# Optimization experiments

Measured on AMD Instinct MI355X. Metric: run time of the kernel, lower is better.

The kernel has to match this reference:

```python
import jax, jax.numpy as jnp
import numpy as np

EMBED_DIM = 1024
NUM_HEADS = 16
LB_HEADS = 8
LA_HEADS = 8
HEAD_DIM = EMBED_DIM // NUM_HEADS


def setup_inputs() -> dict:
    key = jax.random.key(0)
    ks = jax.random.split(key, 8)
    B, T, F, D = 2, 16, 128, EMBED_DIM
    def xavier(k, shape):
        fan_out, fan_in = shape[-2], shape[-1]
        lim = float(np.sqrt(6.0 / (fan_in + fan_out)))
        return jax.random.uniform(k, shape, jnp.float32, -lim, lim)
    return {
        "x": jax.random.normal(ks[0], (B, T, F, D), jnp.float32),
        # stacked per-head Linear weights, torch layout (out=head_dim, in=D)
        "Wq_lb": xavier(ks[1], (LB_HEADS, HEAD_DIM, D)),
        "Wk_lb": xavier(ks[2], (LB_HEADS, HEAD_DIM, D)),
        "Wv_lb": xavier(ks[3], (LB_HEADS, HEAD_DIM, D)),
        "Wq_la": xavier(ks[4], (LA_HEADS, HEAD_DIM, D)),
        "Wk_la": xavier(ks[5], (LA_HEADS, HEAD_DIM, D)),
        "Wv_la": xavier(ks[6], (LA_HEADS, HEAD_DIM, D)),
        "Wo": xavier(ks[7], (D, D)),
    }


def _masked_attention(xf, Wq, Wk, Wv, lookahead):
    # xf: (B, N, D); W*: (H, E, D). Equivalent to per-head Linear then stack.
    q = jnp.einsum('bnd,hed->bhne', xf, Wq)
    k = jnp.einsum('bnd,hed->bhne', xf, Wk)
    v = jnp.einsum('bnd,hed->bhne', xf, Wv)
    scale = 1.0 / jnp.sqrt(jnp.asarray(q.shape[-1], q.dtype))
    s = jnp.einsum('bhqe,bhke->bhqk', q, k) * scale
    n = s.shape[-1]
    i = jnp.arange(n)
    # frame/patch divmod mask reduces to token-level (anti-)causal
    mask = (i[:, None] <= i[None, :]) if lookahead else (i[:, None] >= i[None, :])
    s = jnp.where(mask, s, jnp.finfo(s.dtype).min)
    p = jax.nn.softmax(s, axis=-1)
    return jnp.einsum('bhqk,bhke->bhqe', p, v)  # (B, H, N, E)


def reference(x, Wq_lb, Wk_lb, Wv_lb, Wq_la, Wk_la, Wv_la, Wo):
    B, T, F, D = x.shape
    xf = x.reshape(B, T * F, D)
    o_lb = _masked_attention(xf, Wq_lb, Wk_lb, Wv_lb, lookahead=False)
    o_la = _masked_attention(xf, Wq_la, Wk_la, Wv_la, lookahead=True)
    o = jnp.concatenate([o_lb, o_la], axis=1)          # (B, H, N, E)
    o = o.reshape(B, T * F, D)                          # NOTE: raw reshape, no head transpose (matches torch source)
    out = jnp.einsum('bnd,od->bno', o, Wo)
    return out.reshape(B, T, F, D)
```

## Files before the change

### kernel.cpp

```cpp
#include <hip/hip_runtime.h>
#include <hip/hip_bf16.h>

constexpr int B_    = 2;
constexpr int NTOK  = 2048;
constexpr int D_    = 1024;
constexpr int H_    = 16;
constexpr int E_    = 64;

using bf16_t = __bf16;
using bf16x8 = __attribute__((ext_vector_type(8))) __bf16;
using bf16x4 = __attribute__((ext_vector_type(4))) __bf16;
using f32x4  = __attribute__((ext_vector_type(4))) float;

#define NEG_BIG  (-30000.0f)
#define QSCALE   (0.125f * 1.44269504088896f)

__device__ __forceinline__ void load16_to_lds(const void* g, void* l) {
  __builtin_amdgcn_global_load_lds((const __attribute__((address_space(1))) void*)g,
                                   (__attribute__((address_space(3))) void*)l, 16, 0, 0);
}

__device__ __forceinline__ void stage64_async(const bf16_t* __restrict__ g, int gs,
                                              bf16_t* l, int tid) {
#pragma unroll
  for (int j = 0; j < 2; ++j) {
    int chunk = j * 256 + tid;
    int row = chunk >> 3, cc = chunk & 7;
    int gcc = cc ^ (row & 7);
    load16_to_lds(g + (long)row * gs + gcc * 8, l + chunk * 8);
  }
}

__device__ __forceinline__ void stage128x64_async(const bf16_t* __restrict__ g, int gs,
                                                  bf16_t* l, int tid) {
#pragma unroll
  for (int j = 0; j < 4; ++j) {
    int chunk = j * 256 + tid;
    int row = chunk >> 3, cc = chunk & 7;
    int gcc = cc ^ (row & 7);
    load16_to_lds(g + (long)row * gs + gcc * 8, l + chunk * 8);
  }
}

__device__ __forceinline__ bf16x8 frag_ld(const bf16_t* l, int row, int ks, int half) {
  int cc = (ks * 4 + half) ^ (row & 7);
  return *(const bf16x8*)&l[row * 64 + cc * 8];
}

__device__ __forceinline__ bf16x8 cvt8(f32x4 f0, f32x4 f1) {
  bf16x8 v;
  v[0] = (bf16_t)f0[0]; v[1] = (bf16_t)f0[1]; v[2] = (bf16_t)f0[2]; v[3] = (bf16_t)f0[3];
  v[4] = (bf16_t)f1[0]; v[5] = (bf16_t)f1[1]; v[6] = (bf16_t)f1[2]; v[7] = (bf16_t)f1[3];
  return v;
}

__device__ __forceinline__ bf16x4 cvt4(f32x4 f, float sc) {
  bf16x4 v;
  v[0] = (bf16_t)(f[0] * sc); v[1] = (bf16_t)(f[1] * sc);
  v[2] = (bf16_t)(f[2] * sc); v[3] = (bf16_t)(f[3] * sc);
  return v;
}

__global__ __launch_bounds__(256) void prep_kernel(
    const float* __restrict__ x,
    const float* __restrict__ q0, const float* __restrict__ q1,
    const float* __restrict__ k0, const float* __restrict__ k1,
    const float* __restrict__ v0, const float* __restrict__ v1,
    const float* __restrict__ wo,
    bf16_t* __restrict__ xb, bf16_t* __restrict__ Wb, bf16_t* __restrict__ Wob)
{
  const int bid = blockIdx.x;
  if (bid < 2048) {
    long i = ((long)bid * 256 + threadIdx.x) * 8;
    *(bf16x8*)&xb[i] = cvt8(*(const f32x4*)&x[i], *(const f32x4*)&x[i + 4]);
  } else if (bid < 3584) {
    int rb = bid - 2048;
    int sec = rb >> 5;
    int qkv = sec >> 4, hh = sec & 15;
    const float* s = (qkv == 0) ? (hh < 8 ? q0 : q1)
                   : (qkv == 1) ? (hh < 8 ? k0 : k1)
                                : (hh < 8 ? v0 : v1);
    s += (long)(hh & 7) * (E_ * D_);
    long off = ((long)(rb & 31) * 256 + threadIdx.x) * 8;
    *(bf16x8*)&Wb[(long)sec * (E_ * D_) + off] =
        cvt8(*(const f32x4*)&s[off], *(const f32x4*)&s[off + 4]);
  } else {
    long i = ((long)(bid - 3584) * 256 + threadIdx.x) * 8;
    *(bf16x8*)&Wob[i] = cvt8(*(const f32x4*)&wo[i], *(const f32x4*)&wo[i + 4]);
  }
}

__global__ __launch_bounds__(256) void qkv128_kernel(
    const bf16_t* __restrict__ xb, const bf16_t* __restrict__ Wb,
    bf16_t* __restrict__ Qb, bf16_t* __restrict__ Kb, bf16_t* __restrict__ Vt)
{
  __shared__ __align__(16) bf16_t smem[2 * 128 * 64];
  bf16_t* As = smem;
  bf16_t* Bs = smem + 128 * 64;

  const int tid = threadIdx.x;
  const int wv = tid >> 6, lane = tid & 63, lane16 = lane & 15, half = lane >> 4;
  const int wm = wv >> 1, wn = wv & 1;
  const int mt = blockIdx.x, nt = blockIdx.y;
  const int sec = nt >> 3;

  const bf16_t* Ag = xb + (long)mt * 128 * D_;
  const bf16_t* Bg = Wb + (long)nt * 128 * D_;

  f32x4 acc[4][4] = {};

  if (sec < 2) {
    for (int k0 = 0; k0 < D_; k0 += 64) {
      __syncthreads();
      stage128x64_async(Ag + k0, D_, As, tid);
      stage128x64_async(Bg + k0, D_, Bs, tid);
      __syncthreads();
#pragma unroll
      for (int ks = 0; ks < 2; ++ks) {
        bf16x8 a[4], b[4];
#pragma unroll
        for (int i = 0; i < 4; ++i) a[i] = frag_ld(As, wm * 64 + i * 16 + lane16, ks, half);
#pragma unroll
        for (int i = 0; i < 4; ++i) b[i] = frag_ld(Bs, wn * 64 + i * 16 + lane16, ks, half);
#pragma unroll
        for (int mi = 0; mi < 4; ++mi)
#pragma unroll
          for (int ni = 0; ni < 4; ++ni)
            acc[mi][ni] = __builtin_amdgcn_mfma_f32_16x16x32_bf16(b[ni], a[mi], acc[mi][ni], 0, 0, 0);
      }
    }
  } else {
    for (int k0 = 0; k0 < D_; k0 += 64) {
      __syncthreads();
      stage128x64_async(Ag + k0, D_, As, tid);
      stage128x64_async(Bg + k0, D_, Bs, tid);
      __syncthreads();
#pragma unroll
      for (int ks = 0; ks < 2; ++ks) {
        bf16x8 a[4], b[4];
#pragma unroll
        for (int i = 0; i < 4; ++i) a[i] = frag_ld(As, wm * 64 + i * 16 + lane16, ks, half);
#pragma unroll
        for (int i = 0; i < 4; ++i) b[i] = frag_ld(Bs, wn * 64 + i * 16 + lane16, ks, half);
#pragma unroll
        for (int mi = 0; mi < 4; ++mi)
#pragma unroll
          for (int ni = 0; ni < 4; ++ni)
            acc[mi][ni] = __builtin_amdgcn_mfma_f32_16x16x32_bf16(a[mi], b[ni], acc[mi][ni], 0, 0, 0);
      }
    }
  }

  const int tok0 = mt * 128;
  const int b  = tok0 >> 11;
  const int n0 = tok0 & 2047;

  if (sec < 2) {
    const float qs = (sec == 0) ? QSCALE : 1.0f;
    bf16_t* L = smem + wn * 8192;
    __syncthreads();
#pragma unroll
    for (int mi = 0; mi < 4; ++mi)
#pragma unroll
      for (int ni = 0; ni < 4; ++ni) {
        int tok = wm * 64 + 16 * mi + lane16;
        int cc  = (2 * ni + (half >> 1)) ^ (tok & 7);
        int sub = half & 1;
        *(bf16x4*)&L[tok * 64 + cc * 8 + sub * 4] = cvt4(acc[mi][ni], qs);
      }
    __syncthreads();
    bf16_t* dst = (sec == 0) ? Qb : Kb;
#pragma unroll
    for (int j = 0; j < 8; ++j) {
      int id = j * 256 + tid;
      int c = id >> 10, rem = id & 1023;
      int tok = rem >> 3, ec = rem & 7;
      int scc = ec ^ (tok & 7);
      bf16x8 v = *(const bf16x8*)&smem[c * 8192 + tok * 64 + scc * 8];
      int hh = (nt & 7) * 2 + c;
      *(bf16x8*)&dst[((long)(b * H_ + hh) * NTOK + n0 + tok) * E_ + ec * 8] = v;
    }
  } else {
#pragma unroll
    for (int c = 0; c < 2; ++c) {
      __syncthreads();
      if (wn == c) {
#pragma unroll
        for (int mi = 0; mi < 4; ++mi)
#pragma unroll
          for (int ni = 0; ni < 4; ++ni) {
            int t0v = wm * 64 + 16 * mi + half * 4;
            int e   = 16 * ni + lane16;
            *(bf16x4*)&smem[e * 144 + t0v] = cvt4(acc[mi][ni], 1.0f);
          }
      }
      __syncthreads();
      int hh = (nt & 7) * 2 + c;
      bf16_t* vdst = Vt + ((long)(b * H_ + hh) * E_) * NTOK;
#pragma unroll
      for (int q = 0; q < 4; ++q) {
        int chunk = q * 256 + tid;
        int e = chunk >> 4, toff = (chunk & 15) * 8;
        *(bf16x8*)&vdst[(long)e * NTOK + n0 + toff] = *(const bf16x8*)&smem[e * 144 + toff];
      }
    }
  }
}

__global__ __launch_bounds__(256) void attn_kernel(
    const bf16_t* __restrict__ Qb, const bf16_t* __restrict__ Kb,
    const bf16_t* __restrict__ Vt, bf16_t* __restrict__ Ob)
{
  __shared__ __align__(16) bf16_t Kl[2][64 * 64];
  __shared__ __align__(16) bf16_t Vl[2][64 * 64];
  __shared__ __align__(16) bf16_t Pl[2][64 * 72];

  const int tid = threadIdx.x;
  const int wv = tid >> 6, lane = tid & 63, lane16 = lane & 15, half = lane >> 4;
  const int qp = blockIdx.x, h = blockIdx.y, b = blockIdx.z;
  const bool causal = (h < 8);
  const int qb[2] = { qp, 31 - qp };
  const long bh = (long)(b * H_ + h);
  const int qrow = 16 * wv + lane16;

  bf16x8 qf[2][2];
#pragma unroll
  for (int t = 0; t < 2; ++t) {
    const bf16_t* qg = Qb + (bh * NTOK + (long)qb[t] * 64 + qrow) * E_;
    qf[t][0] = *(const bf16x8*)(qg + half * 8);
    qf[t][1] = *(const bf16x8*)(qg + 32 + half * 8);
  }

  f32x4 oacc[2][4] = {};
  float l_acc[2] = { 0.f, 0.f };

  const int lo = causal ? 0 : qp;
  const int hi = causal ? 31 - qp : 31;

  stage64_async(Kb + (bh * NTOK + (long)lo * 64) * E_, E_, Kl[0], tid);
  stage64_async(Vt + bh * E_ * NTOK + (long)lo * 64, NTOK, Vl[0], tid);

  for (int kb = lo; kb <= hi; ++kb) {
    const int cur = (kb - lo) & 1;
    __syncthreads();
    if (kb < hi) {
      stage64_async(Kb + (bh * NTOK + (long)(kb + 1) * 64) * E_, E_, Kl[cur ^ 1], tid);
      stage64_async(Vt + bh * E_ * NTOK + (long)(kb + 1) * 64, NTOK, Vl[cur ^ 1], tid);
    }
    const bool act[2] = { causal ? (kb <= qb[0]) : (kb >= qb[0]),
                          causal ? (kb <= qb[1]) : (kb >= qb[1]) };

    bf16x8 kfr[2][4];
#pragma unroll
    for (int ks = 0; ks < 2; ++ks)
#pragma unroll
      for (int n = 0; n < 4; ++n)
        kfr[ks][n] = frag_ld(Kl[cur], 16 * n + lane16, ks, half);

#pragma unroll
    for (int t = 0; t < 2; ++t) {
      if (!act[t]) continue;
      f32x4 s[4] = {};
#pragma unroll
      for (int ks = 0; ks < 2; ++ks)
#pragma unroll
        for (int n = 0; n < 4; ++n)
          s[n] = __builtin_amdgcn_mfma_f32_16x16x32_bf16(kfr[ks][n], qf[t][ks], s[n], 0, 0, 0);

      if (kb == qb[t]) {
#pragma unroll
        for (int n = 0; n < 4; ++n)
#pragma unroll
          for (int r = 0; r < 4; ++r) {
            int key = 16 * n + half * 4 + r;
            bool ok = causal ? (qrow >= key) : (qrow <= key);
            s[n][r] = ok ? s[n][r] : NEG_BIG;
          }
      }

      float lsum = 0.f;
#pragma unroll
      for (int n = 0; n < 4; ++n)
#pragma unroll
        for (int r = 0; r < 4; ++r) {
          float p = exp2f(s[n][r]);
          s[n][r] = p;
          lsum += p;
        }
      l_acc[t] += lsum;

#pragma unroll
      for (int n = 0; n < 4; ++n)
        *(bf16x4*)&Pl[t][qrow * 72 + 16 * n + half * 4] = cvt4(s[n], 1.0f);
    }
    asm volatile("" ::: "memory");

    bf16x8 vfr[2][4];
#pragma unroll
    for (int ks = 0; ks < 2; ++ks)
#pragma unroll
      for (int n = 0; n < 4; ++n)
        vfr[ks][n] = frag_ld(Vl[cur], 16 * n + lane16, ks, half);

#pragma unroll
    for (int t = 0; t < 2; ++t) {
      if (!act[t]) continue;
      bf16x8 ap0 = *(const bf16x8*)&Pl[t][qrow * 72 + half * 8];
      bf16x8 ap1 = *(const bf16x8*)&Pl[t][qrow * 72 + 32 + half * 8];
#pragma unroll
      for (int n = 0; n < 4; ++n)
        oacc[t][n] = __builtin_amdgcn_mfma_f32_16x16x32_bf16(vfr[0][n], ap0, oacc[t][n], 0, 0, 0);
#pragma unroll
      for (int n = 0; n < 4; ++n)
        oacc[t][n] = __builtin_amdgcn_mfma_f32_16x16x32_bf16(vfr[1][n], ap1, oacc[t][n], 0, 0, 0);
    }
  }

#pragma unroll
  for (int t = 0; t < 2; ++t) {
    l_acc[t] += __shfl_xor(l_acc[t], 16, 64);
    l_acc[t] += __shfl_xor(l_acc[t], 32, 64);
  }

#pragma unroll
  for (int t = 0; t < 2; ++t) {
    float rcp = 1.0f / l_acc[t];
    bf16_t* og = Ob + (bh * NTOK + (long)qb[t] * 64 + qrow) * E_;
#pragma unroll
    for (int n = 0; n < 4; ++n)
      *(bf16x4*)&og[16 * n + half * 4] = cvt4(oacc[t][n], rcp);
  }
}

__global__ __launch_bounds__(256) void oproj128_kernel(
    const bf16_t* __restrict__ Ob, const bf16_t* __restrict__ Wob,
    float* __restrict__ res)
{
  __shared__ __align__(16) bf16_t smem[2 * 128 * 64];
  bf16_t* As = smem;
  bf16_t* Bs = smem + 128 * 64;

  const int tid = threadIdx.x;
  const int wv = tid >> 6, lane = tid & 63, lane16 = lane & 15, half = lane >> 4;
  const int wm = wv >> 1, wn = wv & 1;
  const int mt = blockIdx.x, nt = blockIdx.y;

  const bf16_t* Ag = Ob  + (long)mt * 128 * D_;
  const bf16_t* Bg = Wob + (long)nt * 128 * D_;

  f32x4 acc[4][4] = {};

  for (int k0 = 0; k0 < D_; k0 += 64) {
    __syncthreads();
    stage128x64_async(Ag + k0, D_, As, tid);
    stage128x64_async(Bg + k0, D_, Bs, tid);
    __syncthreads();
#pragma unroll
    for (int ks = 0; ks < 2; ++ks) {
      bf16x8 a[4], b[4];
#pragma unroll
      for (int i = 0; i < 4; ++i) a[i] = frag_ld(As, wm * 64 + i * 16 + lane16, ks, half);
#pragma unroll
      for (int i = 0; i < 4; ++i) b[i] = frag_ld(Bs, wn * 64 + i * 16 + lane16, ks, half);
#pragma unroll
      for (int mi = 0; mi < 4; ++mi)
#pragma unroll
        for (int ni = 0; ni < 4; ++ni)
          acc[mi][ni] = __builtin_amdgcn_mfma_f32_16x16x32_bf16(b[ni], a[mi], acc[mi][ni], 0, 0, 0);
    }
  }

  float* Lf = (float*)smem;
#pragma unroll
  for (int pass = 0; pass < 2; ++pass) {
    __syncthreads();
    if (wn == pass) {
#pragma unroll
      for (int mi = 0; mi < 4; ++mi)
#pragma unroll
        for (int ni = 0; ni < 4; ++ni) {
          int tok = wm * 64 + 16 * mi + lane16;
          int cc  = (4 * ni + half) ^ (tok & 15);
          *(f32x4*)&Lf[tok * 64 + cc * 4] = acc[mi][ni];
        }
    }
    __syncthreads();
#pragma unroll
    for (int j = 0; j < 8; ++j) {
      int id = j * 256 + tid;
      int tok = id >> 4, c = id & 15;
      int cc = c ^ (tok & 15);
      f32x4 v = *(const f32x4*)&Lf[tok * 64 + cc * 4];
      *(f32x4*)&res[(long)(mt * 128 + tok) * D_ + nt * 128 + pass * 64 + c * 4] = v;
    }
  }
}

__global__ __launch_bounds__(256) void copy_kernel(const float* __restrict__ src,
                                                   float* __restrict__ dst) {
  long i = ((long)blockIdx.x * 256 + threadIdx.x) * 8;
  *(f32x4*)&dst[i]     = *(const f32x4*)&src[i];
  *(f32x4*)&dst[i + 4] = *(const f32x4*)&src[i + 4];
}

extern "C" void kernel_launch(void* const* d_in, const int* in_sizes, int n_in,
                              void* d_out, int out_size, void* d_ws, size_t ws_size,
                              hipStream_t stream) {
  const float* x     = (const float*)d_in[0];
  const float* wq_lb = (const float*)d_in[1];
  const float* wk_lb = (const float*)d_in[2];
  const float* wv_lb = (const float*)d_in[3];
  const float* wq_la = (const float*)d_in[4];
  const float* wk_la = (const float*)d_in[5];
  const float* wv_la = (const float*)d_in[6];
  const float* wo    = (const float*)d_in[7];
  float* out = (float*)d_out;

  const size_t per_buf = (size_t)B_ * H_ * NTOK * E_;

  bf16_t* Qb = (bf16_t*)d_ws;
  bf16_t* Kb = Qb + per_buf;
  bf16_t* Vt = Kb + per_buf;

  bf16_t* xb = (bf16_t*)d_out;
  bf16_t* Wb = xb + per_buf;

  const bool direct = ws_size >= (size_t)34 * 1024 * 1024;

  if (direct) {
    bf16_t* Ob  = Vt + per_buf;
    bf16_t* Wob = Ob + per_buf;
    prep_kernel<<<4096, 256, 0, stream>>>(x, wq_lb, wq_la, wk_lb, wk_la,
                                          wv_lb, wv_la, wo, xb, Wb, Wob);
    qkv128_kernel<<<dim3(32, 24), 256, 0, stream>>>(xb, Wb, Qb, Kb, Vt);
    attn_kernel<<<dim3(16, 16, 2), 256, 0, stream>>>(Qb, Kb, Vt, Ob);
    oproj128_kernel<<<dim3(32, 8), 256, 0, stream>>>(Ob, Wob, out);
  } else {
    bf16_t* Wob = Wb + (size_t)3 * 1024 * 1024;
    bf16_t* Ob  = (bf16_t*)d_out;
    float*  res = (float*)d_ws;
    prep_kernel<<<4096, 256, 0, stream>>>(x, wq_lb, wq_la, wk_lb, wk_la,
                                          wv_lb, wv_la, wo, xb, Wb, Wob);
    qkv128_kernel<<<dim3(32, 24), 256, 0, stream>>>(xb, Wb, Qb, Kb, Vt);
    attn_kernel<<<dim3(16, 16, 2), 256, 0, stream>>>(Qb, Kb, Vt, Ob);
    oproj128_kernel<<<dim3(32, 8), 256, 0, stream>>>(Ob, Wob, res);
    copy_kernel<<<2048, 256, 0, stream>>>(res, out);
  }
}
```

Baseline: 201.4 us.

## Split attention work across key dimension per wave with LDS reduction of partial outputs

Each attention block now handles one 64-query tile instead of a balanced pair, launching twice as many blocks. Within a block, each wave owns 16 keys of the key tile rather than 16 queries, so P stays in registers and feeds 16x16x16 MFMAs directly, with no round trip through LDS. The partial outputs and row sums of the four waves are reduced through a float LDS buffer at the end. This removes the per-iteration P store and reload, at the cost of an end-of-kernel reduction, load imbalance between causal tiles, and smaller MFMA shapes.

```diff
diff --git a/kernel.cpp b/kernel.cpp
--- a/kernel.cpp
+++ b/kernel.cpp
@@ -11,9 +11,21 @@
 using bf16x8 = __attribute__((ext_vector_type(8))) __bf16;
 using bf16x4 = __attribute__((ext_vector_type(4))) __bf16;
 using f32x4  = __attribute__((ext_vector_type(4))) float;
+using s16x4  = __attribute__((ext_vector_type(4))) short;
 
 #define NEG_BIG  (-30000.0f)
 #define QSCALE   (0.125f * 1.44269504088896f)
+
+#if __has_builtin(__builtin_amdgcn_mfma_f32_16x16x16_bf16)
+__device__ __forceinline__ f32x4 mfma16(bf16x4 a, bf16x4 b, f32x4 c) {
+  return __builtin_amdgcn_mfma_f32_16x16x16_bf16(a, b, c, 0, 0, 0);
+}
+#else
+__device__ __forceinline__ f32x4 mfma16(bf16x4 a, bf16x4 b, f32x4 c) {
+  return __builtin_amdgcn_mfma_f32_16x16x16bf16_1k(
+      __builtin_bit_cast(s16x4, a), __builtin_bit_cast(s16x4, b), c, 0, 0, 0);
+}
+#endif
 
 __device__ __forceinline__ void load16_to_lds(const void* g, void* l) {
   __builtin_amdgcn_global_load_lds((const __attribute__((address_space(1))) void*)g,
@@ -207,35 +219,39 @@
   }
 }
 
-__global__ __launch_bounds__(256) void attn_kernel(
+__global__ __launch_bounds__(256, 3) void attn_kernel(
     const bf16_t* __restrict__ Qb, const bf16_t* __restrict__ Kb,
     const bf16_t* __restrict__ Vt, bf16_t* __restrict__ Ob)
 {
   __shared__ __align__(16) bf16_t Kl[2][64 * 64];
   __shared__ __align__(16) bf16_t Vl[2][64 * 64];
-  __shared__ __align__(16) bf16_t Pl[2][64 * 72];
+  __shared__ __align__(16) float  Or[64 * 68];
+  __shared__ float Lr[4][64];
 
   const int tid = threadIdx.x;
   const int wv = tid >> 6, lane = tid & 63, lane16 = lane & 15, half = lane >> 4;
-  const int qp = blockIdx.x, h = blockIdx.y, b = blockIdx.z;
+  const int xb_ = blockIdx.x;
+  const int qb = (xb_ & 1) ? (31 - (xb_ >> 1)) : (xb_ >> 1);
+  const int h = blockIdx.y, b = blockIdx.z;
   const bool causal = (h < 8);
-  const int qb[2] = { qp, 31 - qp };
   const long bh = (long)(b * H_ + h);
-  const int qrow = 16 * wv + lane16;
-
-  bf16x8 qf[2][2];
-#pragma unroll
-  for (int t = 0; t < 2; ++t) {
-    const bf16_t* qg = Qb + (bh * NTOK + (long)qb[t] * 64 + qrow) * E_;
-    qf[t][0] = *(const bf16x8*)(qg + half * 8);
-    qf[t][1] = *(const bf16x8*)(qg + 32 + half * 8);
-  }
-
-  f32x4 oacc[2][4] = {};
-  float l_acc[2] = { 0.f, 0.f };
-
-  const int lo = causal ? 0 : qp;
-  const int hi = causal ? 31 - qp : 31;
+
+  bf16x8 qf[4][2];
+  {
+    const bf16_t* qg = Qb + (bh * NTOK + (long)qb * 64) * E_;
+#pragma unroll
+    for (int qblk = 0; qblk < 4; ++qblk) {
+      const bf16_t* r = qg + (16 * qblk + lane16) * E_;
+      qf[qblk][0] = *(const bf16x8*)(r + half * 8);
+      qf[qblk][1] = *(const bf16x8*)(r + 32 + half * 8);
+    }
+  }
+
+  f32x4 oacc[4][4] = {};
+  float l_acc[4] = {};
+
+  const int lo = causal ? 0 : qb;
+  const int hi = causal ? qb : 31;
 
   stage64_async(Kb + (bh * NTOK + (long)lo * 64) * E_, E_, Kl[0], tid);
   stage64_async(Vt + bh * E_ * NTOK + (long)lo * 64, NTOK, Vl[0], tid);
@@ -247,88 +263,98 @@
       stage64_async(Kb + (bh * NTOK + (long)(kb + 1) * 64) * E_, E_, Kl[cur ^ 1], tid);
       stage64_async(Vt + bh * E_ * NTOK + (long)(kb + 1) * 64, NTOK, Vl[cur ^ 1], tid);
     }
-    const bool act[2] = { causal ? (kb <= qb[0]) : (kb >= qb[0]),
-                          causal ? (kb <= qb[1]) : (kb >= qb[1]) };
-
-    bf16x8 kfr[2][4];
-#pragma unroll
-    for (int ks = 0; ks < 2; ++ks)
-#pragma unroll
-      for (int n = 0; n < 4; ++n)
-        kfr[ks][n] = frag_ld(Kl[cur], 16 * n + lane16, ks, half);
-
-#pragma unroll
-    for (int t = 0; t < 2; ++t) {
-      if (!act[t]) continue;
-      f32x4 s[4] = {};
-#pragma unroll
-      for (int ks = 0; ks < 2; ++ks)
-#pragma unroll
-        for (int n = 0; n < 4; ++n)
-          s[n] = __builtin_amdgcn_mfma_f32_16x16x32_bf16(kfr[ks][n], qf[t][ks], s[n], 0, 0, 0);
-
-      if (kb == qb[t]) {
-#pragma unroll
-        for (int n = 0; n < 4; ++n)
-#pragma unroll
-          for (int r = 0; r < 4; ++r) {
-            int key = 16 * n + half * 4 + r;
-            bool ok = causal ? (qrow >= key) : (qrow <= key);
-            s[n][r] = ok ? s[n][r] : NEG_BIG;
-          }
-      }
-
-      float lsum = 0.f;
-#pragma unroll
-      for (int n = 0; n < 4; ++n)
+
+    bf16x8 kf0 = frag_ld(Kl[cur], 16 * wv + lane16, 0, half);
+    bf16x8 kf1 = frag_ld(Kl[cur], 16 * wv + lane16, 1, half);
+
+    f32x4 s[4] = {};
+#pragma unroll
+    for (int qblk = 0; qblk < 4; ++qblk) {
+      s[qblk] = __builtin_amdgcn_mfma_f32_16x16x32_bf16(kf0, qf[qblk][0], s[qblk], 0, 0, 0);
+      s[qblk] = __builtin_amdgcn_mfma_f32_16x16x32_bf16(kf1, qf[qblk][1], s[qblk], 0, 0, 0);
+    }
+
+    if (kb == qb) {
+#pragma unroll
+      for (int qblk = 0; qblk < 4; ++qblk)
 #pragma unroll
         for (int r = 0; r < 4; ++r) {
-          float p = exp2f(s[n][r]);
-          s[n][r] = p;
-          lsum += p;
+          int key = 16 * wv + 4 * half + r;
+          int q   = 16 * qblk + lane16;
+          bool ok = causal ? (q >= key) : (q <= key);
+          s[qblk][r] = ok ? s[qblk][r] : NEG_BIG;
         }
-      l_acc[t] += lsum;
-
-#pragma unroll
-      for (int n = 0; n < 4; ++n)
-        *(bf16x4*)&Pl[t][qrow * 72 + 16 * n + half * 4] = cvt4(s[n], 1.0f);
-    }
-    asm volatile("" ::: "memory");
-
-    bf16x8 vfr[2][4];
-#pragma unroll
-    for (int ks = 0; ks < 2; ++ks)
-#pragma unroll
-      for (int n = 0; n < 4; ++n)
-        vfr[ks][n] = frag_ld(Vl[cur], 16 * n + lane16, ks, half);
-
-#pragma unroll
-    for (int t = 0; t < 2; ++t) {
-      if (!act[t]) continue;
-      bf16x8 ap0 = *(const bf16x8*)&Pl[t][qrow * 72 + half * 8];
-      bf16x8 ap1 = *(const bf16x8*)&Pl[t][qrow * 72 + 32 + half * 8];
-#pragma unroll
-      for (int n = 0; n < 4; ++n)
-        oacc[t][n] = __builtin_amdgcn_mfma_f32_16x16x32_bf16(vfr[0][n], ap0, oacc[t][n], 0, 0, 0);
-#pragma unroll
-      for (int n = 0; n < 4; ++n)
-        oacc[t][n] = __builtin_amdgcn_mfma_f32_16x16x32_bf16(vfr[1][n], ap1, oacc[t][n], 0, 0, 0);
-    }
-  }
-
-#pragma unroll
-  for (int t = 0; t < 2; ++t) {
-    l_acc[t] += __shfl_xor(l_acc[t], 16, 64);
-    l_acc[t] += __shfl_xor(l_acc[t], 32, 64);
-  }
-
-#pragma unroll
-  for (int t = 0; t < 2; ++t) {
-    float rcp = 1.0f / l_acc[t];
-    bf16_t* og = Ob + (bh * NTOK + (long)qb[t] * 64 + qrow) * E_;
-#pragma unroll
-    for (int n = 0; n < 4; ++n)
-      *(bf16x4*)&og[16 * n + half * 4] = cvt4(oacc[t][n], rcp);
+    }
+
+    bf16x4 pb[4];
+#pragma unroll
+    for (int qblk = 0; qblk < 4; ++qblk) {
+      float ls = 0.f;
+#pragma unroll
+      for (int r = 0; r < 4; ++r) {
+        float p = exp2f(s[qblk][r]);
+        s[qblk][r] = p;
+        ls += p;
+      }
+      l_acc[qblk] += ls;
+      pb[qblk] = cvt4(s[qblk], 1.0f);
+    }
+
+    bf16x4 vf[4];
+#pragma unroll
+    for (int eblk = 0; eblk < 4; ++eblk) {
+      int row = 16 * eblk + lane16;
+      int cc  = (2 * wv + (half >> 1)) ^ (row & 7);
+      vf[eblk] = *(const bf16x4*)&Vl[cur][row * 64 + cc * 8 + (half & 1) * 4];
+    }
+
+#pragma unroll
+    for (int eblk = 0; eblk < 4; ++eblk)
+#pragma unroll
+      for (int qblk = 0; qblk < 4; ++qblk)
+        oacc[eblk][qblk] = mfma16(vf[eblk], pb[qblk], oacc[eblk][qblk]);
+  }
+
+#pragma unroll
+  for (int qblk = 0; qblk < 4; ++qblk) {
+    l_acc[qblk] += __shfl_xor(l_acc[qblk], 16, 64);
+    l_acc[qblk] += __shfl_xor(l_acc[qblk], 32, 64);
+  }
+  if (half == 0) {
+#pragma unroll
+    for (int qblk = 0; qblk < 4; ++qblk)
+      Lr[wv][16 * qblk + lane16] = l_acc[qblk];
+  }
+
+#pragma unroll
+  for (int r = 0; r < 4; ++r) {
+    int qq = (wv + r) & 3;
+#pragma unroll
+    for (int eblk = 0; eblk < 4; ++eblk) {
+      float* p = &Or[(16 * qq + lane16) * 68 + 16 * eblk + 4 * half];
+      if (r == 0) {
+        *(f32x4*)p = oacc[eblk][qq];
+      } else {
+        f32x4 v = *(const f32x4*)p;
+        v += oacc[eblk][qq];
+        *(f32x4*)p = v;
+      }
+    }
+    __syncthreads();
+  }
+
+  {
+    int q = tid >> 2, e0 = (tid & 3) * 16;
+    float l = Lr[0][q] + Lr[1][q] + Lr[2][q] + Lr[3][q];
+    float rcp = 1.0f / l;
+    const float* src = &Or[q * 68 + e0];
+    f32x4 v0 = *(const f32x4*)(src + 0)  * rcp;
+    f32x4 v1 = *(const f32x4*)(src + 4)  * rcp;
+    f32x4 v2 = *(const f32x4*)(src + 8)  * rcp;
+    f32x4 v3 = *(const f32x4*)(src + 12) * rcp;
+    bf16_t* og = Ob + (bh * NTOK + (long)qb * 64 + q) * E_ + e0;
+    *(bf16x8*)(og)     = cvt8(v0, v1);
+    *(bf16x8*)(og + 8) = cvt8(v2, v3);
   }
 }
 
@@ -433,7 +459,7 @@
     prep_kernel<<<4096, 256, 0, stream>>>(x, wq_lb, wq_la, wk_lb, wk_la,
                                           wv_lb, wv_la, wo, xb, Wb, Wob);
     qkv128_kernel<<<dim3(32, 24), 256, 0, stream>>>(xb, Wb, Qb, Kb, Vt);
-    attn_kernel<<<dim3(16, 16, 2), 256, 0, stream>>>(Qb, Kb, Vt, Ob);
+    attn_kernel<<<dim3(32, 16, 2), 256, 0, stream>>>(Qb, Kb, Vt, Ob);
     oproj128_kernel<<<dim3(32, 8), 256, 0, stream>>>(Ob, Wob, out);
   } else {
     bf16_t* Wob = Wb + (size_t)3 * 1024 * 1024;
@@ -442,7 +468,7 @@
     prep_kernel<<<4096, 256, 0, stream>>>(x, wq_lb, wq_la, wk_lb, wk_la,
                                           wv_lb, wv_la, wo, xb, Wb, Wob);
     qkv128_kernel<<<dim3(32, 24), 256, 0, stream>>>(xb, Wb, Qb, Kb, Vt);
-    attn_kernel<<<dim3(16, 16, 2), 256, 0, stream>>>(Qb, Kb, Vt, Ob);
+    attn_kernel<<<dim3(32, 16, 2), 256, 0, stream>>>(Qb, Kb, Vt, Ob);
     oproj128_kernel<<<dim3(32, 8), 256, 0, stream>>>(Ob, Wob, res);
     copy_kernel<<<2048, 256, 0, stream>>>(res, out);
   }
```

New measurement: 439.0 us. +118.0%, slower.
